# Kernel optimization log

Hardware: AMD Instinct MI355X
Metric: run time of the kernel (lower is better)

The kernel has to match this reference:

```python
import jax, jax.numpy as jnp
import numpy as np
import math

B, S, D, H = 2, 2048, 1024, 16
DH = D // H  # dim_per_head = 64


def setup_inputs() -> dict:
    key = jax.random.key(0)
    ks = jax.random.split(key, 12)
    s = 1.0 / math.sqrt(D)
    return {
        "key": jax.random.normal(ks[0], (B, S, D), jnp.float32),
        "value": jax.random.normal(ks[1], (B, S, D), jnp.float32),
        "query": jax.random.normal(ks[2], (B, S, D), jnp.float32),
        "mask": jax.random.randint(ks[3], (B, S, S), 0, 2).astype(bool),
        "Wq": jax.random.normal(ks[4], (D, D), jnp.float32) * s,
        "bq": jnp.zeros((D,), jnp.float32),
        "Wk": jax.random.normal(ks[5], (D, D), jnp.float32) * s,
        "bk": jnp.zeros((D,), jnp.float32),
        "Wv": jax.random.normal(ks[6], (D, D), jnp.float32) * s,
        "bv": jnp.zeros((D,), jnp.float32),
        "Wo": jax.random.normal(ks[7], (D, D), jnp.float32) * s,
        "bo": jnp.zeros((D,), jnp.float32),
    }


def _shape(x):
    # [B, S, D] -> [B, H, S, DH]
    return x.reshape(B, -1, H, DH).transpose(0, 2, 1, 3)


def reference(key, value, query, mask, Wq, bq, Wk, bk, Wv, bv, Wo, bo):
    q = _shape(query @ Wq.T + bq)  # [B,H,Sq,DH]
    k = _shape(key @ Wk.T + bk)    # [B,H,Sk,DH]
    v = _shape(value @ Wv.T + bv)  # [B,H,Sk,DH]
    q = q / jnp.sqrt(jnp.asarray(DH, q.dtype))
    scores = jnp.einsum("bhqd,bhkd->bhqk", q, k)
    scores = jnp.where(mask[:, None, :, :], jnp.asarray(-1e18, scores.dtype), scores)
    attn = jax.nn.softmax(scores, axis=-1)
    # dropout is identity in eval/deterministic reference
    ctx = jnp.einsum("bhqk,bhkd->bhqd", attn, v)
    ctx = ctx.transpose(0, 2, 1, 3).reshape(B, -1, D)  # unshape
    return ctx @ Wo.T + bo
```

## Files before the change

kernel.cpp:

```cpp
#include <hip/hip_runtime.h>
#include <math.h>


constexpr int Bc  = 2;
constexpr int Sc  = 2048;
constexpr int Dc  = 1024;
constexpr int Hc  = 16;
constexpr int DHc = 64;
constexpr int BSc = Bc * Sc;

constexpr float LOG2E = 1.4426950408889634f;

typedef __bf16 bf16x8 __attribute__((ext_vector_type(8)));
typedef __bf16 bf16x4 __attribute__((ext_vector_type(4)));
typedef float  f32x4  __attribute__((ext_vector_type(4)));

#define GLDS16(gp, lp) __builtin_amdgcn_global_load_lds( \
    (const __attribute__((address_space(1))) void*)(gp), \
    (__attribute__((address_space(3))) void*)(lp), 16, 0, 0)

__global__ __launch_bounds__(256)
void wsplit(const float* __restrict__ W0, const float* __restrict__ W1,
            const float* __restrict__ W2, const float* __restrict__ W3,
            __bf16* __restrict__ out)
{
    const float* src[4] = {W0, W1, W2, W3};
    const int z = blockIdx.y;
    const size_t idx = ((size_t)blockIdx.x * 256 + threadIdx.x) * 4;
    const float4 v = *(const float4*)&src[z][idx];
    bf16x4 o;
    o[0] = (__bf16)v.x; o[1] = (__bf16)v.y; o[2] = (__bf16)v.z; o[3] = (__bf16)v.w;
    *(bf16x4*)&out[(size_t)z * Dc * Dc + idx] = o;
}

__device__ __forceinline__ void sweep128p(const float* __restrict__ A,
                                          const __bf16* __restrict__ Wh,
                                          char* AsB, char* WsB,
                                          int gm0, int gn0, f32x4 acc[4][4])
{
    const int tid  = threadIdx.x;
    const int w    = tid >> 6;
    const int lane = tid & 63;
    const int cc   = lane & 15;
    const int g    = lane >> 4;
    const int wm   = (w & 1) * 64;
    const int wn   = (w >> 1) * 64;

    int wrow[4], wchk[4];
#pragma unroll
    for (int r = 0; r < 4; ++r) {
        const int L = r * 256 + tid;
        wrow[r] = L >> 3;
        wchk[r] = (L & 7) ^ (wrow[r] & 7);
    }

    float4 av[8];
#pragma unroll
    for (int r = 0; r < 4; ++r)
        GLDS16(Wh + (size_t)(gn0 + wrow[r]) * Dc + wchk[r] * 8,
               WsB + (r * 256 + tid) * 16);
#pragma unroll
    for (int i = 0; i < 8; ++i) {
        const int Lq = i * 256 + tid;
        av[i] = *(const float4*)&A[(size_t)(gm0 + (Lq >> 4)) * Dc + (Lq & 15) * 4];
    }
#pragma unroll
    for (int i = 0; i < 8; ++i) {
        const int Lq = i * 256 + tid;
        const int ar = Lq >> 4, aq = Lq & 15;
        const int off = ar * 128 + ((((aq >> 1) ^ (ar & 7)) << 4) | ((aq & 1) << 3));
        bf16x4 hv;
        hv[0] = (__bf16)av[i].x; hv[1] = (__bf16)av[i].y;
        hv[2] = (__bf16)av[i].z; hv[3] = (__bf16)av[i].w;
        *(bf16x4*)(AsB + off) = hv;
    }

    for (int it = 0; it < Dc / 64; ++it) {
        const char* As = AsB + (it & 1) * 16384;
        const char* Ws = WsB + (it & 1) * 16384;
        __syncthreads();

        const bool more = (it + 1 < Dc / 64);
        if (more) {
            const int kn = (it + 1) * 64;
            char* Wn = WsB + ((it + 1) & 1) * 16384;
#pragma unroll
            for (int r = 0; r < 4; ++r)
                GLDS16(Wh + (size_t)(gn0 + wrow[r]) * Dc + kn + wchk[r] * 8,
                       Wn + (r * 256 + tid) * 16);
#pragma unroll
            for (int i = 0; i < 8; ++i) {
                const int Lq = i * 256 + tid;
                av[i] = *(const float4*)
                    &A[(size_t)(gm0 + (Lq >> 4)) * Dc + kn + (Lq & 15) * 4];
            }
        }

#pragma unroll
        for (int kk = 0; kk < 2; ++kk) {
            const int cb4 = (kk * 4 + g) << 4;
            bf16x8 af[4], bfr[4];
#pragma unroll
            for (int mt = 0; mt < 4; ++mt) {
                const int row = wm + mt * 16 + cc;
                af[mt] = *(const bf16x8*)(As + row * 128 + (cb4 ^ ((row & 7) << 4)));
            }
#pragma unroll
            for (int nt = 0; nt < 4; ++nt) {
                const int row = wn + nt * 16 + cc;
                bfr[nt] = *(const bf16x8*)(Ws + row * 128 + (cb4 ^ ((row & 7) << 4)));
            }
#pragma unroll
            for (int mt = 0; mt < 4; ++mt)
#pragma unroll
                for (int nt = 0; nt < 4; ++nt)
                    acc[mt][nt] = __builtin_amdgcn_mfma_f32_16x16x32_bf16(
                        af[mt], bfr[nt], acc[mt][nt], 0, 0, 0);
        }

        if (more) {
            char* An = AsB + ((it + 1) & 1) * 16384;
#pragma unroll
            for (int i = 0; i < 8; ++i) {
                const int Lq = i * 256 + tid;
                const int ar = Lq >> 4, aq = Lq & 15;
                const int off = ar * 128 +
                                ((((aq >> 1) ^ (ar & 7)) << 4) | ((aq & 1) << 3));
                bf16x4 hv;
                hv[0] = (__bf16)av[i].x; hv[1] = (__bf16)av[i].y;
                hv[2] = (__bf16)av[i].z; hv[3] = (__bf16)av[i].w;
                *(bf16x4*)(An + off) = hv;
            }
        }
    }
}

__device__ __forceinline__ void sweep64p(const __bf16* __restrict__ Ahi,
                                         const __bf16* __restrict__ Alo,
                                         const __bf16* __restrict__ Wh,
                                         char* WsB, char* AhB, char* AlB,
                                         int gm0, int gn0, f32x4 acc[2][4])
{
    const int tid  = threadIdx.x;
    const int w    = tid >> 6;
    const int lane = tid & 63;
    const int cc   = lane & 15;
    const int g    = lane >> 4;
    const int wm   = (w & 1) * 32;
    const int wn   = (w >> 1) * 64;

    int wrow[4], wchk[4];
#pragma unroll
    for (int r = 0; r < 4; ++r) {
        const int L = r * 256 + tid;
        wrow[r] = L >> 3;
        wchk[r] = (L & 7) ^ (wrow[r] & 7);
    }
    int arow[2], achk[2];
#pragma unroll
    for (int r = 0; r < 2; ++r) {
        const int L = r * 256 + tid;
        arow[r] = L >> 3;
        achk[r] = (L & 7) ^ (arow[r] & 7);
    }

#pragma unroll
    for (int r = 0; r < 4; ++r)
        GLDS16(Wh + (size_t)(gn0 + wrow[r]) * Dc + wchk[r] * 8,
               WsB + (r * 256 + tid) * 16);
#pragma unroll
    for (int r = 0; r < 2; ++r) {
        GLDS16(Ahi + (size_t)(gm0 + arow[r]) * Dc + achk[r] * 8,
               AhB + (r * 256 + tid) * 16);
        GLDS16(Alo + (size_t)(gm0 + arow[r]) * Dc + achk[r] * 8,
               AlB + (r * 256 + tid) * 16);
    }

    for (int it = 0; it < Dc / 64; ++it) {
        const char* Ws = WsB + (it & 1) * 16384;
        const char* Ah = AhB + (it & 1) * 8192;
        const char* Al = AlB + (it & 1) * 8192;
        __syncthreads();

        if (it + 1 < Dc / 64) {
            const int kn = (it + 1) * 64;
            char* Wn = WsB + ((it + 1) & 1) * 16384;
            char* Hn = AhB + ((it + 1) & 1) * 8192;
            char* Ln = AlB + ((it + 1) & 1) * 8192;
#pragma unroll
            for (int r = 0; r < 4; ++r)
                GLDS16(Wh + (size_t)(gn0 + wrow[r]) * Dc + kn + wchk[r] * 8,
                       Wn + (r * 256 + tid) * 16);
#pragma unroll
            for (int r = 0; r < 2; ++r) {
                GLDS16(Ahi + (size_t)(gm0 + arow[r]) * Dc + kn + achk[r] * 8,
                       Hn + (r * 256 + tid) * 16);
                GLDS16(Alo + (size_t)(gm0 + arow[r]) * Dc + kn + achk[r] * 8,
                       Ln + (r * 256 + tid) * 16);
            }
        }

#pragma unroll
        for (int kk = 0; kk < 2; ++kk) {
            const int cb4 = (kk * 4 + g) << 4;
            bf16x8 ahi[2], alo[2], bfr[4];
#pragma unroll
            for (int mt = 0; mt < 2; ++mt) {
                const int row = wm + mt * 16 + cc;
                const int off = row * 128 + (cb4 ^ ((row & 7) << 4));
                ahi[mt] = *(const bf16x8*)(Ah + off);
                alo[mt] = *(const bf16x8*)(Al + off);
            }
#pragma unroll
            for (int nt = 0; nt < 4; ++nt) {
                const int row = wn + nt * 16 + cc;
                bfr[nt] = *(const bf16x8*)(Ws + row * 128 + (cb4 ^ ((row & 7) << 4)));
            }
#pragma unroll
            for (int mt = 0; mt < 2; ++mt)
#pragma unroll
                for (int nt = 0; nt < 4; ++nt) {
                    acc[mt][nt] = __builtin_amdgcn_mfma_f32_16x16x32_bf16(
                        ahi[mt], bfr[nt], acc[mt][nt], 0, 0, 0);
                    acc[mt][nt] = __builtin_amdgcn_mfma_f32_16x16x32_bf16(
                        alo[mt], bfr[nt], acc[mt][nt], 0, 0, 0);
                }
        }
    }
}

__global__ __launch_bounds__(256)
void qkv_mfma(const float* __restrict__ query, const float* __restrict__ key,
              const float* __restrict__ value, const __bf16* __restrict__ Whi,
              const float* __restrict__ bq, const float* __restrict__ bk,
              const float* __restrict__ bv,
              __bf16* __restrict__ Qo, __bf16* __restrict__ Ko, __bf16* __restrict__ Vt)
{
    __shared__ __align__(16) char smem[65536];

    const int z = blockIdx.z;
    const float* A    = (z == 0) ? query : (z == 1) ? key : value;
    const float* bias = (z == 0) ? bq    : (z == 1) ? bk  : bv;
    const float scale = (z == 0) ? 0.125f * LOG2E : 1.0f;
    const __bf16* Wh  = Whi + (size_t)z * Dc * Dc;

    const int gm0 = blockIdx.x * 128;
    const int gn0 = blockIdx.y * 128;

    f32x4 acc[4][4];
#pragma unroll
    for (int mt = 0; mt < 4; ++mt)
#pragma unroll
        for (int nt = 0; nt < 4; ++nt) acc[mt][nt] = {0.f, 0.f, 0.f, 0.f};

    sweep128p(A, Wh, smem, smem + 32768, gm0, gn0, acc);

    const int tid = threadIdx.x;
    const int w = tid >> 6, lane = tid & 63;
    const int cc = lane & 15, g = lane >> 4;
    const int wm = (w & 1) * 64, wn = (w >> 1) * 64;

    float bias4[4];
#pragma unroll
    for (int nt = 0; nt < 4; ++nt) bias4[nt] = bias[gn0 + wn + nt * 16 + cc];

    if (z == 2) {
#pragma unroll
        for (int mt = 0; mt < 4; ++mt)
#pragma unroll
            for (int nt = 0; nt < 4; ++nt) {
                const int col = gn0 + wn + nt * 16 + cc;
                const int h = col >> 6, dh = col & 63;
                const int row0 = gm0 + wm + mt * 16 + g * 4;
                const int b = row0 >> 11, s0 = row0 & 2047;
                bf16x4 vv;
#pragma unroll
                for (int reg = 0; reg < 4; ++reg)
                    vv[reg] = (__bf16)(acc[mt][nt][reg] + bias4[nt]);
                *(bf16x4*)&Vt[(((size_t)(b * Hc + h)) * DHc + dh) * Sc + s0] = vv;
            }
    } else {
        __bf16* O = (z == 0) ? Qo : Ko;
#pragma unroll
        for (int mt = 0; mt < 4; ++mt)
#pragma unroll
            for (int nt = 0; nt < 4; ++nt) {
                const int col = gn0 + wn + nt * 16 + cc;
                const int h = col >> 6, dh = col & 63;
#pragma unroll
                for (int reg = 0; reg < 4; ++reg) {
                    const int row = gm0 + wm + mt * 16 + g * 4 + reg;
                    const int b = row >> 11, s = row & 2047;
                    O[(((size_t)(b * Hc + h)) * Sc + s) * DHc + dh] =
                        (__bf16)((acc[mt][nt][reg] + bias4[nt]) * scale);
                }
            }
    }
}

__global__ __launch_bounds__(256)
void out_mfma(const __bf16* __restrict__ ctxHi, const __bf16* __restrict__ ctxLo,
              const __bf16* __restrict__ Wohi,
              const float* __restrict__ bo, float* __restrict__ out)
{
    __shared__ __align__(16) char smem[65536];

    const int gm0 = blockIdx.x * 64;
    const int gn0 = blockIdx.y * 128;

    f32x4 acc[2][4];
#pragma unroll
    for (int mt = 0; mt < 2; ++mt)
#pragma unroll
        for (int nt = 0; nt < 4; ++nt) acc[mt][nt] = {0.f, 0.f, 0.f, 0.f};

    sweep64p(ctxHi, ctxLo, Wohi, smem, smem + 32768, smem + 49152, gm0, gn0, acc);

    const int tid = threadIdx.x;
    const int w = tid >> 6, lane = tid & 63;
    const int cc = lane & 15, g = lane >> 4;
    const int wm = (w & 1) * 32, wn = (w >> 1) * 64;

    float bias4[4];
#pragma unroll
    for (int nt = 0; nt < 4; ++nt) bias4[nt] = bo[gn0 + wn + nt * 16 + cc];

#pragma unroll
    for (int mt = 0; mt < 2; ++mt)
#pragma unroll
        for (int nt = 0; nt < 4; ++nt) {
            const int col = gn0 + wn + nt * 16 + cc;
#pragma unroll
            for (int reg = 0; reg < 4; ++reg) {
                const int row = gm0 + wm + mt * 16 + g * 4 + reg;
                out[(size_t)row * Dc + col] = acc[mt][nt][reg] + bias4[nt];
            }
        }
}

__global__ __launch_bounds__(256)
void mask_pack(const int* __restrict__ mask, unsigned long long* __restrict__ out)
{
    const int lane = threadIdx.x & 63;
    const size_t waveBase = ((size_t)blockIdx.x * 4 + (threadIdx.x >> 6)) * 256;
    unsigned long long b0 = __ballot(mask[waveBase + lane]        != 0);
    unsigned long long b1 = __ballot(mask[waveBase + 64 + lane]   != 0);
    unsigned long long b2 = __ballot(mask[waveBase + 128 + lane]  != 0);
    unsigned long long b3 = __ballot(mask[waveBase + 192 + lane]  != 0);
    if (lane == 0) {
        unsigned long long* dst = out + (waveBase >> 6);
        dst[0] = b0; dst[1] = b1; dst[2] = b2; dst[3] = b3;
    }
}

__global__ __launch_bounds__(256, 4)
void attn_mfma(const __bf16* __restrict__ Q, const __bf16* __restrict__ K,
               const __bf16* __restrict__ Vt,
               const unsigned long long* __restrict__ mp,
               __bf16* __restrict__ ctxHi, __bf16* __restrict__ ctxLo)
{
    __shared__ __align__(16) char smem[40960];

    const int tid  = threadIdx.x;
    const int w    = tid >> 6;
    const int lane = tid & 63;
    const int cc   = lane & 15;
    const int g    = lane >> 4;
    const int bh   = blockIdx.y;
    const int b    = bh >> 4;
    const int h    = bh & 15;
    const int qw   = blockIdx.x * 64 + w * 16;

    const __bf16* Qb  = Q  + (size_t)bh * Sc * DHc;
    const __bf16* Kb  = K  + (size_t)bh * Sc * DHc;
    const __bf16* Vtb = Vt + (size_t)bh * DHc * Sc;

    char* Pw = smem + 32768 + w * 2048;

    bf16x8 qa[2];
    qa[0] = *(const bf16x8*)&Qb[(size_t)(qw + cc) * DHc + g * 8];
    qa[1] = *(const bf16x8*)&Qb[(size_t)(qw + cc) * DHc + 32 + g * 8];

    f32x4 o[4] = {};
    float l[4] = {};

    const int ci[2] = {tid, 256 + tid};
    int  rowi[2], ski[2], krow[2];
#pragma unroll
    for (int i = 0; i < 2; ++i) {
        rowi[i] = ci[i] >> 3;
        const int sl = ci[i] & 7;
        ski[i]  = sl ^ (rowi[i] & 7);
        krow[i] = ((rowi[i] & 15) << 2) | (rowi[i] >> 4);
    }

    const int pswW = ((( (g * 4) ^ ((g * 4) >> 3)) & 7) << 4);
    const int pswR = (((cc ^ (cc >> 3)) & 7) << 4);

#pragma unroll
    for (int i = 0; i < 2; ++i) {
        GLDS16(Kb + (size_t)krow[i] * DHc + ski[i] * 8,
               smem + ci[i] * 16);
        GLDS16(Vtb + (size_t)rowi[i] * Sc + ski[i] * 8,
               smem + 8192 + ci[i] * 16);
    }

    for (int it = 0; it < 32; ++it) {
        const int k0 = it * 64;
        char* Ks = smem + (it & 1) * 16384;
        char* Vs = Ks + 8192;

        __syncthreads();

        if (it + 1 < 32) {
            char* Kn = smem + ((it + 1) & 1) * 16384;
            const int kn = k0 + 64;
#pragma unroll
            for (int i = 0; i < 2; ++i) {
                GLDS16(Kb + (size_t)(kn + krow[i]) * DHc + ski[i] * 8,
                       Kn + ci[i] * 16);
                GLDS16(Vtb + (size_t)rowi[i] * Sc + kn + ski[i] * 8,
                       Kn + 8192 + ci[i] * 16);
            }
        }

        unsigned long long mw[4];
#pragma unroll
        for (int r = 0; r < 4; ++r)
            mw[r] = mp[(size_t)(b * Sc + qw + g * 4 + r) * (Sc / 64) + (k0 >> 6)];

        f32x4 sc[4];
#pragma unroll
        for (int nt = 0; nt < 4; ++nt) {
            const int row = nt * 16 + cc;
            const int rx  = (row & 7) << 4;
            const bf16x8 kb0 = *(const bf16x8*)(Ks + row * 128 + ((g << 4) ^ rx));
            const bf16x8 kb1 = *(const bf16x8*)(Ks + row * 128 + ((64 + (g << 4)) ^ rx));
            f32x4 z = {-24.f, -24.f, -24.f, -24.f};
            z = __builtin_amdgcn_mfma_f32_16x16x32_bf16(qa[0], kb0, z, 0, 0, 0);
            z = __builtin_amdgcn_mfma_f32_16x16x32_bf16(qa[1], kb1, z, 0, 0, 0);
            sc[nt] = z;
        }

        bf16x8 pa[2];
#pragma unroll
        for (int r = 0; r < 4; ++r) {
            const unsigned s4 = (unsigned)(mw[r] >> (cc * 4)) & 0xFu;
            bf16x4 pv;
#pragma unroll
            for (int nt = 0; nt < 4; ++nt) {
                float p = __builtin_amdgcn_exp2f(sc[nt][r]);
                p = (s4 & (1u << nt)) ? 0.f : p;
                l[r] += p;
                pv[nt] = (__bf16)p;
            }
            const int prow = g * 4 + r;
            const int psw  = (((prow ^ (prow >> 3)) & 7) << 4);
            *(bf16x4*)(Pw + prow * 128 + ((8 * cc) ^ psw)) = pv;
        }
        pa[0] = *(const bf16x8*)(Pw + cc * 128 + ((16 * g) ^ pswR));
        pa[1] = *(const bf16x8*)(Pw + cc * 128 + ((64 + 16 * g) ^ pswR));

#pragma unroll
        for (int nt = 0; nt < 4; ++nt) {
            const int row = nt * 16 + cc;
            const int rx  = (row & 7) << 4;
            const bf16x8 vb0 = *(const bf16x8*)(Vs + row * 128 + ((g << 4) ^ rx));
            const bf16x8 vb1 = *(const bf16x8*)(Vs + row * 128 + ((64 + (g << 4)) ^ rx));
            o[nt] = __builtin_amdgcn_mfma_f32_16x16x32_bf16(pa[0], vb0, o[nt], 0, 0, 0);
            o[nt] = __builtin_amdgcn_mfma_f32_16x16x32_bf16(pa[1], vb1, o[nt], 0, 0, 0);
        }
    }

    (void)pswW;

#pragma unroll
    for (int off = 1; off < 16; off <<= 1)
#pragma unroll
        for (int r = 0; r < 4; ++r)
            l[r] += __shfl_xor(l[r], off, 16);

#pragma unroll
    for (int r = 0; r < 4; ++r) {
        const float inv = 1.0f / l[r];
        const int q = qw + g * 4 + r;
#pragma unroll
        for (int nt = 0; nt < 4; ++nt) {
            const size_t idx = ((size_t)b * Sc + q) * Dc + h * 64 + nt * 16 + cc;
            const float v = o[nt][r] * inv;
            const __bf16 hi = (__bf16)v;
            ctxHi[idx] = hi;
            ctxLo[idx] = (__bf16)(v - (float)hi);
        }
    }
}

extern "C" void kernel_launch(void* const* d_in, const int* in_sizes, int n_in,
                              void* d_out, int out_size, void* d_ws, size_t ws_size,
                              hipStream_t stream)
{
    const float* key   = (const float*)d_in[0];
    const float* value = (const float*)d_in[1];
    const float* query = (const float*)d_in[2];
    const int*   mask  = (const int*)  d_in[3];
    const float* Wq    = (const float*)d_in[4];
    const float* bq    = (const float*)d_in[5];
    const float* Wk    = (const float*)d_in[6];
    const float* bk    = (const float*)d_in[7];
    const float* Wv    = (const float*)d_in[8];
    const float* bv    = (const float*)d_in[9];
    const float* Wo    = (const float*)d_in[10];
    const float* bo    = (const float*)d_in[11];
    float* out = (float*)d_out;

    char* wsb = (char*)d_ws;
    __bf16* Qbf  = (__bf16*)(wsb);
    __bf16* Kbf  = (__bf16*)(wsb + ((size_t)8  << 20));
    __bf16* Vt   = (__bf16*)(wsb + ((size_t)16 << 20));
    unsigned long long* mpk = (unsigned long long*)(wsb + ((size_t)32 << 20));
    __bf16* Whi  = (__bf16*)(wsb + ((size_t)33 << 20));
    __bf16* ctxHi = (__bf16*)(wsb + ((size_t)41 << 20));
    __bf16* ctxLo = (__bf16*)(wsb + ((size_t)49 << 20));

    dim3 gws(Dc * Dc / (256 * 4), 4);
    wsplit<<<gws, 256, 0, stream>>>(Wq, Wk, Wv, Wo, Whi);

    dim3 gqkv(BSc / 128, Dc / 128, 3);
    qkv_mfma<<<gqkv, 256, 0, stream>>>(query, key, value, Whi, bq, bk, bv,
                                       Qbf, Kbf, Vt);

    const int mask_n = Bc * Sc * Sc;
    mask_pack<<<mask_n / 1024, 256, 0, stream>>>(mask, mpk);

    dim3 gattn(Sc / 64, Bc * Hc);
    attn_mfma<<<gattn, 256, 0, stream>>>(Qbf, Kbf, Vt, mpk, ctxHi, ctxLo);

    dim3 gout(BSc / 64, Dc / 128);
    out_mfma<<<gout, 256, 0, stream>>>(ctxHi, ctxLo, Whi + (size_t)3 * Dc * Dc,
                                       bo, out);
}
```

Before: 280.0 us.

## Switch attention to 32x32x16 MFMA with in-register P via permlane32 swap

Rewrites the attention kernel to use 32x32x16 bf16 MFMAs with 32 queries per wave and 128 per block. The score tile is computed transposed (K as A operand), so P can be rebuilt as the A operand for PV in registers with permlane32_swap, with no LDS round trip. This halves K/V tile reloads per query and adds s_setprio around the MFMA bursts. In exchange it lowers occupancy (launch bounds 2, fewer blocks) and raises register pressure with the f32x16 accumulators.

```diff
diff --git a/kernel.cpp b/kernel.cpp
--- a/kernel.cpp
+++ b/kernel.cpp
@@ -13,7 +13,11 @@
 
 typedef __bf16 bf16x8 __attribute__((ext_vector_type(8)));
 typedef __bf16 bf16x4 __attribute__((ext_vector_type(4)));
+typedef __bf16 bf16x2 __attribute__((ext_vector_type(2)));
 typedef float  f32x4  __attribute__((ext_vector_type(4)));
+typedef float  f32x16 __attribute__((ext_vector_type(16)));
+typedef unsigned uint32x2 __attribute__((ext_vector_type(2)));
+typedef unsigned uint32x4 __attribute__((ext_vector_type(4)));
 
 #define GLDS16(gp, lp) __builtin_amdgcn_global_load_lds( \
     (const __attribute__((address_space(1))) void*)(gp), \
@@ -353,146 +357,163 @@
     }
 }
 
-__global__ __launch_bounds__(256, 4)
+__global__ __launch_bounds__(256, 2)
 void attn_mfma(const __bf16* __restrict__ Q, const __bf16* __restrict__ K,
                const __bf16* __restrict__ Vt,
                const unsigned long long* __restrict__ mp,
                __bf16* __restrict__ ctxHi, __bf16* __restrict__ ctxLo)
 {
-    __shared__ __align__(16) char smem[40960];
+    __shared__ __align__(16) char smem[32768];
 
     const int tid  = threadIdx.x;
     const int w    = tid >> 6;
     const int lane = tid & 63;
-    const int cc   = lane & 15;
-    const int g    = lane >> 4;
+    const int c    = lane & 31;
+    const int u    = lane >> 5;
     const int bh   = blockIdx.y;
     const int b    = bh >> 4;
     const int h    = bh & 15;
-    const int qw   = blockIdx.x * 64 + w * 16;
+    const int qw   = blockIdx.x * 128 + w * 32;
 
     const __bf16* Qb  = Q  + (size_t)bh * Sc * DHc;
     const __bf16* Kb  = K  + (size_t)bh * Sc * DHc;
     const __bf16* Vtb = Vt + (size_t)bh * DHc * Sc;
 
-    char* Pw = smem + 32768 + w * 2048;
-
-    bf16x8 qa[2];
-    qa[0] = *(const bf16x8*)&Qb[(size_t)(qw + cc) * DHc + g * 8];
-    qa[1] = *(const bf16x8*)&Qb[(size_t)(qw + cc) * DHc + 32 + g * 8];
-
-    f32x4 o[4] = {};
-    float l[4] = {};
+    bf16x8 qa[4];
+#pragma unroll
+    for (int ch = 0; ch < 4; ++ch)
+        qa[ch] = *(const bf16x8*)&Qb[(size_t)(qw + c) * DHc + ch * 16 + u * 8];
+
+    f32x16 o[2];
+#pragma unroll
+    for (int dt = 0; dt < 2; ++dt)
+#pragma unroll
+        for (int i = 0; i < 16; ++i) o[dt][i] = 0.f;
+    float lp[4] = {0.f, 0.f, 0.f, 0.f};
 
     const int ci[2] = {tid, 256 + tid};
-    int  rowi[2], ski[2], krow[2];
+    int rowi[2], ski[2];
 #pragma unroll
     for (int i = 0; i < 2; ++i) {
         rowi[i] = ci[i] >> 3;
-        const int sl = ci[i] & 7;
-        ski[i]  = sl ^ (rowi[i] & 7);
-        krow[i] = ((rowi[i] & 15) << 2) | (rowi[i] >> 4);
-    }
-
-    const int pswW = ((( (g * 4) ^ ((g * 4) >> 3)) & 7) << 4);
-    const int pswR = (((cc ^ (cc >> 3)) & 7) << 4);
+        ski[i]  = (ci[i] & 7) ^ (rowi[i] & 7);
+    }
 
 #pragma unroll
     for (int i = 0; i < 2; ++i) {
-        GLDS16(Kb + (size_t)krow[i] * DHc + ski[i] * 8,
+        GLDS16(Kb + (size_t)rowi[i] * DHc + ski[i] * 8,
                smem + ci[i] * 16);
         GLDS16(Vtb + (size_t)rowi[i] * Sc + ski[i] * 8,
                smem + 8192 + ci[i] * 16);
     }
 
     for (int it = 0; it < 32; ++it) {
-        const int k0 = it * 64;
-        char* Ks = smem + (it & 1) * 16384;
-        char* Vs = Ks + 8192;
+        const char* Ks = smem + (it & 1) * 16384;
+        const char* Vs = Ks + 8192;
 
         __syncthreads();
 
         if (it + 1 < 32) {
             char* Kn = smem + ((it + 1) & 1) * 16384;
-            const int kn = k0 + 64;
+            const int kn = (it + 1) * 64;
 #pragma unroll
             for (int i = 0; i < 2; ++i) {
-                GLDS16(Kb + (size_t)(kn + krow[i]) * DHc + ski[i] * 8,
+                GLDS16(Kb + (size_t)(kn + rowi[i]) * DHc + ski[i] * 8,
                        Kn + ci[i] * 16);
                 GLDS16(Vtb + (size_t)rowi[i] * Sc + kn + ski[i] * 8,
                        Kn + 8192 + ci[i] * 16);
             }
         }
 
-        unsigned long long mw[4];
-#pragma unroll
-        for (int r = 0; r < 4; ++r)
-            mw[r] = mp[(size_t)(b * Sc + qw + g * 4 + r) * (Sc / 64) + (k0 >> 6)];
-
-        f32x4 sc[4];
-#pragma unroll
-        for (int nt = 0; nt < 4; ++nt) {
-            const int row = nt * 16 + cc;
-            const int rx  = (row & 7) << 4;
-            const bf16x8 kb0 = *(const bf16x8*)(Ks + row * 128 + ((g << 4) ^ rx));
-            const bf16x8 kb1 = *(const bf16x8*)(Ks + row * 128 + ((64 + (g << 4)) ^ rx));
-            f32x4 z = {-24.f, -24.f, -24.f, -24.f};
-            z = __builtin_amdgcn_mfma_f32_16x16x32_bf16(qa[0], kb0, z, 0, 0, 0);
-            z = __builtin_amdgcn_mfma_f32_16x16x32_bf16(qa[1], kb1, z, 0, 0, 0);
+        const unsigned long long mw =
+            mp[((size_t)(b * Sc + qw + c) << 5) + it];
+
+        f32x16 sc[2];
+        __builtin_amdgcn_s_setprio(1);
+#pragma unroll
+        for (int nt = 0; nt < 2; ++nt) {
+            f32x16 z;
+#pragma unroll
+            for (int i = 0; i < 16; ++i) z[i] = -24.f;
+#pragma unroll
+            for (int ch = 0; ch < 4; ++ch) {
+                const int row = nt * 32 + c;
+                const bf16x8 kb = *(const bf16x8*)
+                    (Ks + row * 128 + ((ch * 32 + u * 16) ^ ((row & 7) << 4)));
+                z = __builtin_amdgcn_mfma_f32_32x32x16_bf16(kb, qa[ch], z, 0, 0, 0);
+            }
             sc[nt] = z;
         }
-
-        bf16x8 pa[2];
-#pragma unroll
-        for (int r = 0; r < 4; ++r) {
-            const unsigned s4 = (unsigned)(mw[r] >> (cc * 4)) & 0xFu;
-            bf16x4 pv;
-#pragma unroll
-            for (int nt = 0; nt < 4; ++nt) {
-                float p = __builtin_amdgcn_exp2f(sc[nt][r]);
-                p = (s4 & (1u << nt)) ? 0.f : p;
-                l[r] += p;
-                pv[nt] = (__bf16)p;
-            }
-            const int prow = g * 4 + r;
-            const int psw  = (((prow ^ (prow >> 3)) & 7) << 4);
-            *(bf16x4*)(Pw + prow * 128 + ((8 * cc) ^ psw)) = pv;
-        }
-        pa[0] = *(const bf16x8*)(Pw + cc * 128 + ((16 * g) ^ pswR));
-        pa[1] = *(const bf16x8*)(Pw + cc * 128 + ((64 + 16 * g) ^ pswR));
-
-#pragma unroll
-        for (int nt = 0; nt < 4; ++nt) {
-            const int row = nt * 16 + cc;
-            const int rx  = (row & 7) << 4;
-            const bf16x8 vb0 = *(const bf16x8*)(Vs + row * 128 + ((g << 4) ^ rx));
-            const bf16x8 vb1 = *(const bf16x8*)(Vs + row * 128 + ((64 + (g << 4)) ^ rx));
-            o[nt] = __builtin_amdgcn_mfma_f32_16x16x32_bf16(pa[0], vb0, o[nt], 0, 0, 0);
-            o[nt] = __builtin_amdgcn_mfma_f32_16x16x32_bf16(pa[1], vb1, o[nt], 0, 0, 0);
-        }
-    }
-
-    (void)pswW;
-
-#pragma unroll
-    for (int off = 1; off < 16; off <<= 1)
-#pragma unroll
-        for (int r = 0; r < 4; ++r)
-            l[r] += __shfl_xor(l[r], off, 16);
-
-#pragma unroll
-    for (int r = 0; r < 4; ++r) {
-        const float inv = 1.0f / l[r];
-        const int q = qw + g * 4 + r;
-#pragma unroll
-        for (int nt = 0; nt < 4; ++nt) {
-            const size_t idx = ((size_t)b * Sc + q) * Dc + h * 64 + nt * 16 + cc;
-            const float v = o[nt][r] * inv;
+        __builtin_amdgcn_s_setprio(0);
+
+        unsigned pk[2][4][2];
+#pragma unroll
+        for (int nt = 0; nt < 2; ++nt)
+#pragma unroll
+            for (int rr = 0; rr < 4; ++rr) {
+                const unsigned nib =
+                    (unsigned)(mw >> (nt * 32 + rr * 8 + u * 4)) & 0xFu;
+                float pv[4];
+#pragma unroll
+                for (int r = 0; r < 4; ++r) {
+                    float p = __builtin_amdgcn_exp2f(sc[nt][rr * 4 + r]);
+                    p = (nib & (1u << r)) ? 0.f : p;
+                    lp[rr] += p;
+                    pv[r] = p;
+                }
+                bf16x2 t0; t0[0] = (__bf16)pv[0]; t0[1] = (__bf16)pv[1];
+                bf16x2 t1; t1[0] = (__bf16)pv[2]; t1[1] = (__bf16)pv[3];
+                pk[nt][rr][0] = __builtin_bit_cast(unsigned, t0);
+                pk[nt][rr][1] = __builtin_bit_cast(unsigned, t1);
+            }
+
+        bf16x8 pa[4];
+#pragma unroll
+        for (int kc = 0; kc < 4; ++kc) {
+            const int nt = kc >> 1;
+            const int r0 = (kc & 1) * 2;
+            uint32x2 s0 = __builtin_amdgcn_permlane32_swap(
+                pk[nt][r0][0], pk[nt][r0 + 1][0], false, false);
+            uint32x2 s1 = __builtin_amdgcn_permlane32_swap(
+                pk[nt][r0][1], pk[nt][r0 + 1][1], false, false);
+            uint32x4 wds;
+            wds[0] = s0[0]; wds[1] = s1[0]; wds[2] = s0[1]; wds[3] = s1[1];
+            pa[kc] = __builtin_bit_cast(bf16x8, wds);
+        }
+
+        __builtin_amdgcn_s_setprio(1);
+#pragma unroll
+        for (int dt = 0; dt < 2; ++dt)
+#pragma unroll
+            for (int kc = 0; kc < 4; ++kc) {
+                const int row = dt * 32 + c;
+                const bf16x8 vb = *(const bf16x8*)
+                    (Vs + row * 128 + ((kc * 32 + u * 16) ^ ((row & 7) << 4)));
+                o[dt] = __builtin_amdgcn_mfma_f32_32x32x16_bf16(pa[kc], vb, o[dt], 0, 0, 0);
+            }
+        __builtin_amdgcn_s_setprio(0);
+    }
+
+    float lsum = (lp[0] + lp[1]) + (lp[2] + lp[3]);
+    lsum += __shfl_xor(lsum, 32);
+    const float linv = 1.0f / lsum;
+
+    float inv[16];
+#pragma unroll
+    for (int i = 0; i < 16; ++i)
+        inv[i] = __shfl(linv, (i & 3) + 8 * (i >> 2) + 4 * u);
+
+#pragma unroll
+    for (int dt = 0; dt < 2; ++dt)
+#pragma unroll
+        for (int i = 0; i < 16; ++i) {
+            const int q = qw + (i & 3) + 8 * (i >> 2) + 4 * u;
+            const size_t idx = ((size_t)b * Sc + q) * Dc + h * 64 + dt * 32 + c;
+            const float v = o[dt][i] * inv[i];
             const __bf16 hi = (__bf16)v;
             ctxHi[idx] = hi;
             ctxLo[idx] = (__bf16)(v - (float)hi);
         }
-    }
 }
 
 extern "C" void kernel_launch(void* const* d_in, const int* in_sizes, int n_in,
@@ -532,7 +553,7 @@
     const int mask_n = Bc * Sc * Sc;
     mask_pack<<<mask_n / 1024, 256, 0, stream>>>(mask, mpk);
 
-    dim3 gattn(Sc / 64, Bc * Hc);
+    dim3 gattn(Sc / 128, Bc * Hc);
     attn_mfma<<<gattn, 256, 0, stream>>>(Qbf, Kbf, Vt, mpk, ctxHi, ctxLo);
 
     dim3 gout(BSc / 64, Dc / 128);
```

New measurement: 272.8 us. 1.03x faster.
